# Performance work log

Measured on AMD Instinct MI355X. Metric: run time of the kernel, lower is better.

The kernel has to match this reference:

```python
import jax, jax.numpy as jnp
import numpy as np

B, IC, H, W = 8, 16, 32, 32
OC, KH, KW = 32, 3, 3
PAD, K = 1, 2
OH, OW = H, W  # stride 1, pad 1, dilation 1 with 3x3 kernel
TABLES = OC * IC * KH * KW  # 4608, one LUT per (oc, ic, kh, kw)
M = TABLES * K              # 9216 mask rows
NUM_ENTRIES = 2 ** K


def setup_inputs() -> dict:
    key = jax.random.key(0)
    k1, k2, k3, k4, k5 = jax.random.split(key, 5)
    inp = jax.random.normal(k1, (B, IC, H, W), dtype=jnp.float32)
    w_luts = jax.random.normal(k2, (TABLES, NUM_ENTRIES), dtype=jnp.float32)
    mask_c = jax.random.randint(k3, (M,), 0, IC)
    mask_kh = jax.random.randint(k4, (M,), 0, KH)
    mask_kw = jax.random.randint(k5, (M,), 0, KW)
    return {"input": inp, "w_luts": w_luts, "mask_c": mask_c,
            "mask_kh": mask_kh, "mask_kw": mask_kw}


def _truth_table():
    # tt[j, i] in {-1, +1}: sign of bit j of truth-table entry i
    entries = jnp.arange(NUM_ENTRIES)
    bits = (entries[None, :] >> jnp.arange(K)[:, None]) & 1  # (K, 2^K)
    return (2 * bits - 1).astype(jnp.float32)


def reference(input, w_luts, mask_c, mask_kh, mask_kw):
    # Fused unfold (im2col) + per-table input_mask gather: instead of
    # materializing folded_input (B, L, IC, KH, KW), gather straight from the
    # padded image: expanded[b, oh, ow, m] = padded[b, c_m, oh + kh_m, ow + kw_m]
    padded = jnp.pad(input, ((0, 0), (0, 0), (PAD, PAD), (PAD, PAD)))
    row = jnp.arange(OH)[:, None] + mask_kh[None, :]   # (OH, M)
    col = jnp.arange(OW)[:, None] + mask_kw[None, :]   # (OW, M)
    expanded = padded[:, mask_c[None, None, :], row[:, None, :], col[None, :, :]]  # (B, OH, OW, M)

    # LagrangeTrainer: per-table soft LUT lookup via Lagrange interpolation
    x = expanded.reshape(B * OH * OW, TABLES, K)
    tt = _truth_table()                                       # (K, 2^K)
    factors = (1.0 + x[..., :, None] * tt[None, None]) * 0.5  # (N, T, K, 2^K)
    basis = jnp.prod(factors, axis=-2)                        # (N, T, 2^K)
    out = jnp.einsum('nte,te->nt', basis, w_luts)             # (N, TABLES)

    # Fold-style reshape + sum over the IC*KH*KW tables feeding each output
    out = out.reshape(B, OC, OH, OW, -1).sum(-1)
    out = out.reshape(B, OH * OW, OC).swapaxes(1, 2).reshape(B, OC, OH, OW)
    return out
```

## Files before the change

### kernel.cpp

```cpp
#include <hip/hip_runtime.h>

#define OC_ 32
#define IC_ 16
#define H_ 32
#define W_ 32
#define B_ 8
#define TPO 144

#define ROWS_PER_WG 16
#define TR 18
#define TC 34
#define CH_STRIDE (TR * TC)
#define TILE_F (IC_ * CH_STRIDE)

struct alignas(16) Rec4 { unsigned offs; float bb, cc, dd; };

__global__ __launch_bounds__(256)
void conv_kernel(const float* __restrict__ input,
                 const float* __restrict__ w_luts,
                 const int*   __restrict__ mask_c,
                 const int*   __restrict__ mask_kh,
                 const int*   __restrict__ mask_kw,
                 float*       __restrict__ out) {
    __shared__ float tile[TILE_F];
    __shared__ Rec4  srec[TPO];
    __shared__ float sAA[TPO];
    __shared__ float sP[8];

    const int oh0 = blockIdx.x * ROWS_PER_WG;
    const int oc  = blockIdx.y;
    const int b   = blockIdx.z;
    const int tid = threadIdx.x;

    if (tid < TPO) {
        int t = oc * TPO + tid;
        const float4 w = *reinterpret_cast<const float4*>(w_luts + 4 * t);
        int m0 = 2 * t, m1 = m0 + 1;
        unsigned off0 = (unsigned)(mask_c[m0] * CH_STRIDE + mask_kh[m0] * TC + mask_kw[m0]) * 4u;
        unsigned off1 = (unsigned)(mask_c[m1] * CH_STRIDE + mask_kh[m1] * TC + mask_kw[m1]) * 4u;
        Rec4 r;
        r.offs = off0 | (off1 << 16);
        r.bb = 0.25f * (-w.x + w.y - w.z + w.w);
        r.cc = 0.25f * (-w.x - w.y + w.z + w.w);
        r.dd = 0.25f * ( w.x - w.y - w.z + w.w);
        srec[tid] = r;
        sAA[tid]  = 0.25f * (w.x + w.y + w.z + w.w);
    }

    const float* inb = input + b * (IC_ * H_ * W_);
    for (int u = tid; u < IC_ * TR * 8; u += 256) {
        int ch  = u / (TR * 8);
        int rem = u - ch * (TR * 8);
        int r   = rem >> 3;
        int c4  = (rem & 7) * 4;
        int grow = oh0 + r - 1;
        float4 v = make_float4(0.f, 0.f, 0.f, 0.f);
        if ((unsigned)grow < (unsigned)H_)
            v = *reinterpret_cast<const float4*>(inb + (ch * H_ + grow) * W_ + c4);
        float* dst = &tile[ch * CH_STRIDE + r * TC + 1 + c4];
        dst[0] = v.x; dst[1] = v.y; dst[2] = v.z; dst[3] = v.w;
    }
    for (int i = tid; i < IC_ * TR * 2; i += 256) {
        int ch  = i / (TR * 2);
        int rem = i - ch * (TR * 2);
        int r   = rem >> 1;
        int cc2 = (rem & 1) ? (TC - 1) : 0;
        tile[ch * CH_STRIDE + r * TC + cc2] = 0.f;
    }
    __syncthreads();

    if (tid < 8) {
        float s = 0.f;
        #pragma unroll
        for (int i = 0; i < 18; ++i) s += sAA[tid * 18 + i];
        sP[tid] = s;
    }
    __syncthreads();
    const float bias = ((sP[0] + sP[1]) + (sP[2] + sP[3]))
                     + ((sP[4] + sP[5]) + (sP[6] + sP[7]));

    const int rl = tid >> 5;
    const int ow = tid & 31;
    const char* tb = (const char*)tile + ((2 * rl) * TC + ow) * 4;
    const int4* sq = reinterpret_cast<const int4*>(srec);

    float accA = 0.f, accB = 0.f;
    #pragma unroll 8
    for (int t = 0; t < TPO; ++t) {
        const int4 q = sq[t];
        const unsigned offs = (unsigned)q.x;
        const float* g0 = reinterpret_cast<const float*>(tb + (offs & 0xffffu));
        const float* g1 = reinterpret_cast<const float*>(tb + (offs >> 16));
        const float x0a = g0[0];
        const float x0b = g0[TC];
        const float x1a = g1[0];
        const float x1b = g1[TC];
        const float bb = __int_as_float(q.y);
        const float cc = __int_as_float(q.z);
        const float dd = __int_as_float(q.w);
        accA = fmaf(bb, x0a, accA);
        accA = fmaf(x1a, fmaf(dd, x0a, cc), accA);
        accB = fmaf(bb, x0b, accB);
        accB = fmaf(x1b, fmaf(dd, x0b, cc), accB);
    }

    const int ohA = oh0 + 2 * rl;
    out[((b * OC_ + oc) * H_ + ohA    ) * W_ + ow] = accA + bias;
    out[((b * OC_ + oc) * H_ + ohA + 1) * W_ + ow] = accB + bias;
}

extern "C" void kernel_launch(void* const* d_in, const int* in_sizes, int n_in,
                              void* d_out, int out_size, void* d_ws, size_t ws_size,
                              hipStream_t stream) {
    const float* input   = (const float*)d_in[0];
    const float* w_luts  = (const float*)d_in[1];
    const int*   mask_c  = (const int*)d_in[2];
    const int*   mask_kh = (const int*)d_in[3];
    const int*   mask_kw = (const int*)d_in[4];
    float* out = (float*)d_out;

    conv_kernel<<<dim3(H_ / ROWS_PER_WG, OC_, B_), dim3(256), 0, stream>>>(
        input, w_luts, mask_c, mask_kh, mask_kw, out);
}
```

Measured before the change: 71.68 us.

## Split table loop across four thread groups with shared-memory reduction

Each workgroup now uses 1024 threads. Four groups of 256 each process a quarter of the 144 tables for the same output positions, and partial sums are combined through shared memory before the store. This raises wave occupancy per CU so the LDS-gather latency of the table loop can be hidden, since the grid has only about two workgroups per CU. The cost is extra shared memory for the reduction buffers, an extra barrier, and an idle epilogue for three quarters of the threads.

```diff
diff --git a/kernel.cpp b/kernel.cpp
--- a/kernel.cpp
+++ b/kernel.cpp
@@ -13,9 +13,13 @@
 #define CH_STRIDE (TR * TC)
 #define TILE_F (IC_ * CH_STRIDE)
 
+#define NQ 4
+#define TQ (TPO / NQ)
+#define NTHR 1024
+
 struct alignas(16) Rec4 { unsigned offs; float bb, cc, dd; };
 
-__global__ __launch_bounds__(256)
+__global__ __launch_bounds__(NTHR, 8)
 void conv_kernel(const float* __restrict__ input,
                  const float* __restrict__ w_luts,
                  const int*   __restrict__ mask_c,
@@ -26,6 +30,8 @@
     __shared__ Rec4  srec[TPO];
     __shared__ float sAA[TPO];
     __shared__ float sP[8];
+    __shared__ float redA[NTHR];
+    __shared__ float redB[NTHR];
 
     const int oh0 = blockIdx.x * ROWS_PER_WG;
     const int oc  = blockIdx.y;
@@ -48,7 +54,7 @@
     }
 
     const float* inb = input + b * (IC_ * H_ * W_);
-    for (int u = tid; u < IC_ * TR * 8; u += 256) {
+    for (int u = tid; u < IC_ * TR * 8; u += NTHR) {
         int ch  = u / (TR * 8);
         int rem = u - ch * (TR * 8);
         int r   = rem >> 3;
@@ -60,7 +66,7 @@
         float* dst = &tile[ch * CH_STRIDE + r * TC + 1 + c4];
         dst[0] = v.x; dst[1] = v.y; dst[2] = v.z; dst[3] = v.w;
     }
-    for (int i = tid; i < IC_ * TR * 2; i += 256) {
+    for (int i = tid; i < IC_ * TR * 2; i += NTHR) {
         int ch  = i / (TR * 2);
         int rem = i - ch * (TR * 2);
         int r   = rem >> 1;
@@ -75,18 +81,18 @@
         for (int i = 0; i < 18; ++i) s += sAA[tid * 18 + i];
         sP[tid] = s;
     }
-    __syncthreads();
-    const float bias = ((sP[0] + sP[1]) + (sP[2] + sP[3]))
-                     + ((sP[4] + sP[5]) + (sP[6] + sP[7]));
 
-    const int rl = tid >> 5;
-    const int ow = tid & 31;
+    const int pos = tid & 255;
+    const int qt  = tid >> 8;
+    const int rl  = pos >> 5;
+    const int ow  = pos & 31;
     const char* tb = (const char*)tile + ((2 * rl) * TC + ow) * 4;
     const int4* sq = reinterpret_cast<const int4*>(srec);
 
     float accA = 0.f, accB = 0.f;
-    #pragma unroll 8
-    for (int t = 0; t < TPO; ++t) {
+    const int t0 = qt * TQ;
+    #pragma unroll 6
+    for (int t = t0; t < t0 + TQ; ++t) {
         const int4 q = sq[t];
         const unsigned offs = (unsigned)q.x;
         const float* g0 = reinterpret_cast<const float*>(tb + (offs & 0xffffu));
@@ -103,10 +109,19 @@
         accB = fmaf(bb, x0b, accB);
         accB = fmaf(x1b, fmaf(dd, x0b, cc), accB);
     }
+    redA[tid] = accA;
+    redB[tid] = accB;
+    __syncthreads();
 
-    const int ohA = oh0 + 2 * rl;
-    out[((b * OC_ + oc) * H_ + ohA    ) * W_ + ow] = accA + bias;
-    out[((b * OC_ + oc) * H_ + ohA + 1) * W_ + ow] = accB + bias;
+    if (tid < 256) {
+        const float bias = ((sP[0] + sP[1]) + (sP[2] + sP[3]))
+                         + ((sP[4] + sP[5]) + (sP[6] + sP[7]));
+        float a = (redA[tid] + redA[tid + 256]) + (redA[tid + 512] + redA[tid + 768]);
+        float bsum = (redB[tid] + redB[tid + 256]) + (redB[tid + 512] + redB[tid + 768]);
+        const int ohA = oh0 + 2 * rl;
+        out[((b * OC_ + oc) * H_ + ohA    ) * W_ + ow] = a + bias;
+        out[((b * OC_ + oc) * H_ + ohA + 1) * W_ + ow] = bsum + bias;
+    }
 }
 
 extern "C" void kernel_launch(void* const* d_in, const int* in_sizes, int n_in,
@@ -119,6 +134,6 @@
     const int*   mask_kw = (const int*)d_in[4];
     float* out = (float*)d_out;
 
-    conv_kernel<<<dim3(H_ / ROWS_PER_WG, OC_, B_), dim3(256), 0, stream>>>(
+    conv_kernel<<<dim3(H_ / ROWS_PER_WG, OC_, B_), dim3(NTHR), 0, stream>>>(
         input, w_luts, mask_c, mask_kh, mask_kw, out);
 }
```

After: 70.24 us. -2.0%, faster.
